# Performance work log

Hardware: AMD Instinct MI355X
Metric: run time of the kernel (lower is better)

## Reference

```python
import jax, jax.numpy as jnp
import numpy as np


def _dwconv(x, w, pad):
    # depthwise conv, NCHW, weight (C,1,kh,kw), feature_group_count=C
    return jax.lax.conv_general_dilated(
        x, w, window_strides=(1, 1), padding=pad,
        feature_group_count=x.shape[1],
        dimension_numbers=('NCHW', 'OIHW', 'NCHW'))


def _max_channel_relu(x):
    # assumed MaxChannelReLU: keep only the channel-max value at each (b,h,w)
    return x * (x == jnp.max(x, axis=1, keepdims=True))


def setup_inputs() -> dict:
    key = jax.random.key(0)
    ks = jax.random.split(key, 6)
    B, C, H, W = 16, 64, 128, 128
    x = jax.random.normal(ks[0], (B, C, H, W), dtype=jnp.float32)
    w_bbx = 0.1 * jax.random.normal(ks[1], (C, 1, 1, 1), dtype=jnp.float32)
    w_width = 0.1 * jax.random.normal(ks[2], (C, 1, 1, 11), dtype=jnp.float32)
    w_width_sh = 0.1 * jax.random.normal(ks[3], (C, 1, 1, 1), dtype=jnp.float32)
    w_height = 0.1 * jax.random.normal(ks[4], (C, 1, 11, 1), dtype=jnp.float32)
    w_height_sh = 0.1 * jax.random.normal(ks[5], (C, 1, 1, 1), dtype=jnp.float32)
    return {"x": x, "w_bbx": w_bbx, "w_width": w_width,
            "w_width_sh": w_width_sh, "w_height": w_height,
            "w_height_sh": w_height_sh}


def reference(x, w_bbx, w_width, w_width_sh, w_height, w_height_sh):
    B, C, H, W = x.shape
    # self.bbx: depthwise 1x1 conv == per-channel scale
    wh = x * w_bbx.reshape(1, C, 1, 1)
    # width branch: depthwise (1,11) conv pad 5, scaled by W, then shared 1x1
    w = _dwconv(wh, w_width, [(0, 0), (5, 5)]) * W
    w = w * w_width_sh.reshape(1, C, 1, 1)
    # height branch: depthwise (11,1) conv pad 5, scaled by H, then shared 1x1
    h = _dwconv(wh, w_height, [(5, 5), (0, 0)]) * H
    h = h * w_height_sh.reshape(1, C, 1, 1)
    sx = jax.nn.sigmoid(x)
    M = jnp.max(sx, axis=(-2, -1), keepdims=True) - 0.01
    score = x * (sx > M).astype(x.dtype)
    S = jnp.sum(score, axis=(-2, -1), keepdims=True)
    sn = score / S  # normalized weights, reused by all weighted reductions
    ws = jnp.sum(w * sn, axis=(-2, -1))
    hs = jnp.sum(h * sn, axis=(-2, -1))
    ps = jnp.max(sx, axis=(-2, -1))
    col = jnp.arange(W, dtype=x.dtype).reshape(1, 1, 1, W)
    row = jnp.arange(H, dtype=x.dtype).reshape(1, 1, H, 1)
    x1 = jnp.sum(col * sn, axis=(-2, -1)) - ws / 2
    y1 = jnp.sum(row * sn, axis=(-2, -1)) - hs / 2
    x2 = x1 + ws
    y2 = y1 + hs
    score_m = _max_channel_relu(score)
    w_m = _max_channel_relu(w)
    h_m = _max_channel_relu(h)
    i = jnp.broadcast_to(jnp.arange(B, dtype=x.dtype)[:, None], (B, C))
    bbox = jnp.stack([i, x1, y1, x2, y2, ps], axis=-1).reshape(-1, 6)
    return jnp.concatenate([score_m, w_m, h_m], axis=1), bbox
```

## Files before the change

kernel.cpp:

```cpp
#include <hip/hip_runtime.h>
#include <math.h>

#define BATCH 16
#define CH    64
#define HH    128
#define WW    128
#define PLANE (HH*WW)
#define OUT0  (BATCH*3*CH*PLANE)
#define BP    (BATCH*PLANE)

#define T_OFF   0
#define PS_OFF  1024
#define SUM_OFF 2048
#define CW_OFF  12288
#define CHS_OFF 12352
#define MAP_OFF 16384
#define FMAP_OFF 3163136

__device__ __forceinline__ float4 fmax4(float4 a, float4 b) {
    float4 r;
    r.x = fmaxf(a.x, b.x); r.y = fmaxf(a.y, b.y);
    r.z = fmaxf(a.z, b.z); r.w = fmaxf(a.w, b.w);
    return r;
}

template <int ROWS, class F>
__device__ __forceinline__ void conv_strip(const float* __restrict__ base,
                                           const float* __restrict__ wk,
                                           const float* __restrict__ hk,
                                           float cw, float chs, float T,
                                           F&& emit) {
    float4 rb[11];
#pragma unroll
    for (int r = 0; r < 11; r++)
        rb[r] = *(const float4*)(base + r * 144 + 8);
#pragma unroll
    for (int j = 0; j < ROWS; j++) {
        if (j > 0)
            rb[(j + 10) % 11] = *(const float4*)(base + (j + 10) * 144 + 8);
        float hx = 0.f, hy = 0.f, hz = 0.f, hw = 0.f;
#pragma unroll
        for (int k = 0; k < 11; k++) {
            float4 v = rb[(j + k) % 11];
            hx = fmaf(v.x, hk[k], hx);
            hy = fmaf(v.y, hk[k], hy);
            hz = fmaf(v.z, hk[k], hz);
            hw = fmaf(v.w, hk[k], hw);
        }
        float4 vx = rb[(j + 5) % 11];
        float wbuf[20];
        {
            const float* row = base + (j + 5) * 144;
            float4 a0 = *(const float4*)(row + 0);
            float4 a1 = *(const float4*)(row + 4);
            float4 a3 = *(const float4*)(row + 12);
            float4 a4 = *(const float4*)(row + 16);
            wbuf[0] = a0.x;  wbuf[1] = a0.y;  wbuf[2] = a0.z;  wbuf[3] = a0.w;
            wbuf[4] = a1.x;  wbuf[5] = a1.y;  wbuf[6] = a1.z;  wbuf[7] = a1.w;
            wbuf[8] = vx.x;  wbuf[9] = vx.y;  wbuf[10] = vx.z; wbuf[11] = vx.w;
            wbuf[12] = a3.x; wbuf[13] = a3.y; wbuf[14] = a3.z; wbuf[15] = a3.w;
            wbuf[16] = a4.x; wbuf[17] = a4.y; wbuf[18] = a4.z; wbuf[19] = a4.w;
        }
        float wo[4];
#pragma unroll
        for (int q = 0; q < 4; q++) {
            float acc = 0.f;
#pragma unroll
            for (int k = 0; k < 11; k++) acc = fmaf(wbuf[q + 3 + k], wk[k], acc);
            wo[q] = acc * cw;
        }
        float4 w4, h4, s4;
        w4.x = wo[0]; w4.y = wo[1]; w4.z = wo[2]; w4.w = wo[3];
        h4.x = hx * chs; h4.y = hy * chs; h4.z = hz * chs; h4.w = hw * chs;
        s4.x = (vx.x > T) ? vx.x : 0.f;
        s4.y = (vx.y > T) ? vx.y : 0.f;
        s4.z = (vx.z > T) ? vx.z : 0.f;
        s4.w = (vx.w > T) ? vx.w : 0.f;
        emit(j, w4, h4, s4);
    }
}

__global__ __launch_bounds__(256) void k_max(const float* __restrict__ x,
                                             const float* __restrict__ w_bbx,
                                             const float* __restrict__ w_width_sh,
                                             const float* __restrict__ w_height_sh,
                                             float* __restrict__ ws) {
    int bid = blockIdx.x;
    const float4* xp = (const float4*)(x + (size_t)bid * PLANE);
    int tid = threadIdx.x;
    float m = -INFINITY;
#pragma unroll
    for (int i = 0; i < 16; i++) {
        float4 v = xp[i * 256 + tid];
        m = fmaxf(m, fmaxf(fmaxf(v.x, v.y), fmaxf(v.z, v.w)));
    }
#pragma unroll
    for (int off = 32; off; off >>= 1) m = fmaxf(m, __shfl_xor(m, off, 64));
    __shared__ float sm[4];
    int wid = tid >> 6, lane = tid & 63;
    if (lane == 0) sm[wid] = m;
    __syncthreads();
    if (tid == 0) {
        float mm = fmaxf(fmaxf(sm[0], sm[1]), fmaxf(sm[2], sm[3]));
        float ps = 1.0f / (1.0f + expf(-mm));
        float M = ps - 0.01f;
        float T = (M > 0.0f) ? logf(M / (1.0f - M)) : -INFINITY;
        ws[T_OFF + bid] = T;
        ws[PS_OFF + bid] = ps;
    }
    if (bid < 64 && tid == 1) {
        float cb = w_bbx[bid];
        ws[CW_OFF + bid]  = 128.0f * w_width_sh[bid] * cb;
        ws[CHS_OFF + bid] = 128.0f * w_height_sh[bid] * cb;
    }
}

__global__ __launch_bounds__(256) void k_cmax(const float* __restrict__ x,
                                              const float* __restrict__ w_width,
                                              const float* __restrict__ w_height,
                                              float* __restrict__ ws) {
    __shared__ float xs[4 * 18 * 144];
    int bid = blockIdx.x;
    int band = bid & 15;
    int cg   = (bid >> 4) & 3;
    int b    = bid >> 6;
    int r0 = band * 8;
    int tid = threadIdx.x;
    int cs = tid & 31;
    int rs = (tid >> 5) & 1;
    int ig = tid >> 6;
    int slot = tid & 63;

    float4* xs4 = (float4*)xs;
    for (int i = tid; i < 4 * 18 * 36; i += 256)
        xs4[i] = make_float4(0.f, 0.f, 0.f, 0.f);

    float4 mw[4], mh[4], ms[4];
#pragma unroll
    for (int j = 0; j < 4; j++) {
        mw[j] = make_float4(-INFINITY, -INFINITY, -INFINITY, -INFINITY);
        mh[j] = mw[j];
        ms[j] = mw[j];
    }

    for (int chunk = 0; chunk < 4; chunk++) {
        int ch0 = cg * 16 + chunk * 4;
        __syncthreads();
        for (int j = tid; j < 4 * 576; j += 256) {
            int i = j / 576;
            int rem = j - i * 576;
            int lr = rem >> 5;
            int c4 = rem & 31;
            int gr = r0 - 5 + lr;
            if (gr >= 0 && gr < 128)
                *(float4*)(xs + (i * 18 + lr) * 144 + 8 + c4 * 4) =
                    *(const float4*)(x +
                        ((size_t)((b * 64 + ch0 + i) * 128 + gr)) * 128 + c4 * 4);
        }
        __syncthreads();
        int c = ch0 + ig;
        float T   = ws[T_OFF + b * 64 + c];
        float cwv = ws[CW_OFF + c];
        float chsv= ws[CHS_OFF + c];
        float wk[11], hk[11];
#pragma unroll
        for (int k = 0; k < 11; k++) {
            wk[k] = w_width[c * 11 + k];
            hk[k] = w_height[c * 11 + k];
        }
        const float* basep = xs + (ig * 18 + rs * 4) * 144 + cs * 4;
        conv_strip<4>(basep, wk, hk, cwv, chsv, T,
            [&](int j, float4 w4, float4 h4, float4 s4) {
                mw[j] = fmax4(mw[j], w4);
                mh[j] = fmax4(mh[j], h4);
                ms[j] = fmax4(ms[j], s4);
            });
    }
    __syncthreads();
    float4* cb = (float4*)xs;
    if (ig > 0) {
#pragma unroll
        for (int j = 0; j < 4; j++) {
            cb[((ig - 1) * 64 + slot) * 12 + j]     = mw[j];
            cb[((ig - 1) * 64 + slot) * 12 + 4 + j] = mh[j];
            cb[((ig - 1) * 64 + slot) * 12 + 8 + j] = ms[j];
        }
    }
    __syncthreads();
    if (ig == 0) {
#pragma unroll
        for (int g = 0; g < 3; g++) {
#pragma unroll
            for (int j = 0; j < 4; j++) {
                mw[j] = fmax4(mw[j], cb[(g * 64 + slot) * 12 + j]);
                mh[j] = fmax4(mh[j], cb[(g * 64 + slot) * 12 + 4 + j]);
                ms[j] = fmax4(ms[j], cb[(g * 64 + slot) * 12 + 8 + j]);
            }
        }
        int pbase = b * PLANE + (r0 + rs * 4) * 128 + cs * 4;
#pragma unroll
        for (int j = 0; j < 4; j++) {
            *(float4*)(ws + MAP_OFF + (size_t)(cg * 3 + 0) * BP + pbase + j * 128) = mw[j];
            *(float4*)(ws + MAP_OFF + (size_t)(cg * 3 + 1) * BP + pbase + j * 128) = mh[j];
            *(float4*)(ws + MAP_OFF + (size_t)(cg * 3 + 2) * BP + pbase + j * 128) = ms[j];
        }
    }
}

__global__ __launch_bounds__(256) void k_combine(float* __restrict__ ws) {
    int id = blockIdx.x * 256 + threadIdx.x;
    int f = id >> 16;
    int r = id & 65535;
    float4 m = *(const float4*)(ws + MAP_OFF + (size_t)f * BP + (size_t)r * 4);
#pragma unroll
    for (int g = 1; g < 4; g++) {
        float4 v = *(const float4*)(ws + MAP_OFF + (size_t)(g * 3 + f) * BP + (size_t)r * 4);
        m = fmax4(m, v);
    }
    *(float4*)(ws + FMAP_OFF + (size_t)f * BP + (size_t)r * 4) = m;
}

__global__ __launch_bounds__(256) void k_write(
    const float* __restrict__ x,
    const float* __restrict__ w_width, const float* __restrict__ w_height,
    float* __restrict__ ws, float* __restrict__ out) {
    __shared__ float xs[74 * 144];
    __shared__ float red[4 * 5];
    int bid = blockIdx.x;
    int half = bid & 1;
    int plane = bid >> 1;
    int b = plane >> 6, c = plane & 63;
    int r0 = half * 64;
    int tid = threadIdx.x;
    int cs = tid & 31;
    int rs = tid >> 5;

    float4* xs4 = (float4*)xs;
    for (int i = tid; i < 74 * 36; i += 256) xs4[i] = make_float4(0.f, 0.f, 0.f, 0.f);
    __syncthreads();
    const float* xp = x + (size_t)plane * PLANE;
    for (int j = tid; j < 74 * 32; j += 256) {
        int br = j >> 5, c4 = j & 31;
        int gr = r0 - 5 + br;
        if (gr >= 0 && gr < 128)
            *(float4*)&xs[br * 144 + 8 + c4 * 4] =
                *(const float4*)(xp + gr * 128 + c4 * 4);
    }
    float wk[11], hk[11];
#pragma unroll
    for (int k = 0; k < 11; k++) {
        wk[k] = w_width[c * 11 + k];
        hk[k] = w_height[c * 11 + k];
    }
    float T   = ws[T_OFF + plane];
    float cwv = ws[CW_OFF + c];
    float chsv= ws[CHS_OFF + c];
    __syncthreads();

    float S = 0.f, Sw = 0.f, Sh = 0.f, Scol = 0.f, Srow = 0.f;
    float* outS = out + (size_t)(b * 192 + c) * PLANE + r0 * 128;
    float* outW = out + (size_t)(b * 192 + 64 + c) * PLANE + r0 * 128;
    float* outH = out + (size_t)(b * 192 + 128 + c) * PLANE + r0 * 128;
    const float* mwp = ws + FMAP_OFF + 0 * (size_t)BP + b * PLANE + r0 * 128;
    const float* mhp = ws + FMAP_OFF + 1 * (size_t)BP + b * PLANE + r0 * 128;
    const float* msp = ws + FMAP_OFF + 2 * (size_t)BP + b * PLANE + r0 * 128;

    const float* basep = xs + (rs * 8) * 144 + cs * 4;
    conv_strip<8>(basep, wk, hk, cwv, chsv, T,
        [&](int j, float4 w4, float4 h4, float4 s4) {
            int ly = rs * 8 + j;
            int p = ly * 128 + cs * 4;
            float s4sum = s4.x + s4.y + s4.z + s4.w;
            S += s4sum;
            Srow += (float)(r0 + ly) * s4sum;
            Sw = fmaf(w4.x, s4.x, Sw); Sw = fmaf(w4.y, s4.y, Sw);
            Sw = fmaf(w4.z, s4.z, Sw); Sw = fmaf(w4.w, s4.w, Sw);
            Sh = fmaf(h4.x, s4.x, Sh); Sh = fmaf(h4.y, s4.y, Sh);
            Sh = fmaf(h4.z, s4.z, Sh); Sh = fmaf(h4.w, s4.w, Sh);
            int xc = cs * 4;
            Scol = fmaf((float)(xc + 0), s4.x, Scol);
            Scol = fmaf((float)(xc + 1), s4.y, Scol);
            Scol = fmaf((float)(xc + 2), s4.z, Scol);
            Scol = fmaf((float)(xc + 3), s4.w, Scol);

            float4 mw = *(const float4*)(mwp + p);
            float4 mh = *(const float4*)(mhp + p);
            float4 msv = *(const float4*)(msp + p);
            float4 o;
            o.x = (s4.x == msv.x) ? s4.x : 0.f;
            o.y = (s4.y == msv.y) ? s4.y : 0.f;
            o.z = (s4.z == msv.z) ? s4.z : 0.f;
            o.w = (s4.w == msv.w) ? s4.w : 0.f;
            *(float4*)(outS + p) = o;
            o.x = (w4.x == mw.x) ? w4.x : 0.f;
            o.y = (w4.y == mw.y) ? w4.y : 0.f;
            o.z = (w4.z == mw.z) ? w4.z : 0.f;
            o.w = (w4.w == mw.w) ? w4.w : 0.f;
            *(float4*)(outW + p) = o;
            o.x = (h4.x == mh.x) ? h4.x : 0.f;
            o.y = (h4.y == mh.y) ? h4.y : 0.f;
            o.z = (h4.z == mh.z) ? h4.z : 0.f;
            o.w = (h4.w == mh.w) ? h4.w : 0.f;
            *(float4*)(outH + p) = o;
        });
#pragma unroll
    for (int off = 32; off; off >>= 1) {
        S    += __shfl_xor(S, off, 64);
        Sw   += __shfl_xor(Sw, off, 64);
        Sh   += __shfl_xor(Sh, off, 64);
        Scol += __shfl_xor(Scol, off, 64);
        Srow += __shfl_xor(Srow, off, 64);
    }
    int wid = tid >> 6, lane = tid & 63;
    if (lane == 0) {
        red[wid * 5 + 0] = S;   red[wid * 5 + 1] = Sw;
        red[wid * 5 + 2] = Sh;  red[wid * 5 + 3] = Scol;
        red[wid * 5 + 4] = Srow;
    }
    __syncthreads();
    if (tid == 0) {
        float a0 = 0, a1 = 0, a2 = 0, a3 = 0, a4 = 0;
#pragma unroll
        for (int w2 = 0; w2 < 4; w2++) {
            a0 += red[w2 * 5 + 0]; a1 += red[w2 * 5 + 1];
            a2 += red[w2 * 5 + 2]; a3 += red[w2 * 5 + 3];
            a4 += red[w2 * 5 + 4];
        }
        int base = SUM_OFF + half * 5120;
        ws[base + 0 * 1024 + plane] = a0;
        ws[base + 1 * 1024 + plane] = a1;
        ws[base + 2 * 1024 + plane] = a2;
        ws[base + 3 * 1024 + plane] = a3;
        ws[base + 4 * 1024 + plane] = a4;
    }
}

__global__ __launch_bounds__(256) void k_bbox(const float* __restrict__ ws,
                                              float* __restrict__ out) {
    int idx = blockIdx.x * 256 + threadIdx.x;
    if (idx >= 1024) return;
    int b = idx >> 6;
    float S    = ws[SUM_OFF + 0 * 1024 + idx] + ws[SUM_OFF + 5120 + 0 * 1024 + idx];
    float Sw   = ws[SUM_OFF + 1 * 1024 + idx] + ws[SUM_OFF + 5120 + 1 * 1024 + idx];
    float Sh   = ws[SUM_OFF + 2 * 1024 + idx] + ws[SUM_OFF + 5120 + 2 * 1024 + idx];
    float Scol = ws[SUM_OFF + 3 * 1024 + idx] + ws[SUM_OFF + 5120 + 3 * 1024 + idx];
    float Srow = ws[SUM_OFF + 4 * 1024 + idx] + ws[SUM_OFF + 5120 + 4 * 1024 + idx];
    float ps   = ws[PS_OFF + idx];
    float inv = 1.0f / S;
    float wsv = Sw * inv, hsv = Sh * inv;
    float x1 = Scol * inv - 0.5f * wsv;
    float y1 = Srow * inv - 0.5f * hsv;
    float* o = out + OUT0 + (size_t)idx * 6;
    o[0] = (float)b;
    o[1] = x1;
    o[2] = y1;
    o[3] = x1 + wsv;
    o[4] = y1 + hsv;
    o[5] = ps;
}

extern "C" void kernel_launch(void* const* d_in, const int* in_sizes, int n_in,
                              void* d_out, int out_size, void* d_ws, size_t ws_size,
                              hipStream_t stream) {
    const float* x          = (const float*)d_in[0];
    const float* w_bbx      = (const float*)d_in[1];
    const float* w_width    = (const float*)d_in[2];
    const float* w_width_sh = (const float*)d_in[3];
    const float* w_height   = (const float*)d_in[4];
    const float* w_height_sh= (const float*)d_in[5];
    float* out = (float*)d_out;
    float* ws  = (float*)d_ws;

    k_max<<<dim3(1024), dim3(256), 0, stream>>>(x, w_bbx, w_width_sh, w_height_sh, ws);
    k_cmax<<<dim3(1024), dim3(256), 0, stream>>>(x, w_width, w_height, ws);
    k_combine<<<dim3(768), dim3(256), 0, stream>>>(ws);
    k_write<<<dim3(2048), dim3(256), 0, stream>>>(x, w_width, w_height, ws, out);
    k_bbox<<<dim3(4), dim3(256), 0, stream>>>(ws, out);
}
```

Before: 323.8 us.

## Fuse channel-max combine and bbox computation into the write kernel

Removes the separate combine kernel by having the write kernel take the max over the four partial channel-group maps directly. It also removes the bbox kernel by using an atomic block counter so the last finishing write block computes the bbox outputs. This saves two launches and the intermediate combined-map write and read. In exchange, every write block reads four times as much map data, and completion ordering now depends on threadfence plus an atomic counter.

```diff
diff --git a/kernel.cpp b/kernel.cpp
--- a/kernel.cpp
+++ b/kernel.cpp
@@ -14,8 +14,8 @@
 #define SUM_OFF 2048
 #define CW_OFF  12288
 #define CHS_OFF 12352
+#define CNT_OFF 12416
 #define MAP_OFF 16384
-#define FMAP_OFF 3163136
 
 __device__ __forceinline__ float4 fmax4(float4 a, float4 b) {
     float4 r;
@@ -113,6 +113,8 @@
         ws[CW_OFF + bid]  = 128.0f * w_width_sh[bid] * cb;
         ws[CHS_OFF + bid] = 128.0f * w_height_sh[bid] * cb;
     }
+    if (bid == 0 && tid == 2)
+        ((unsigned int*)ws)[CNT_OFF] = 0u;
 }
 
 __global__ __launch_bounds__(256) void k_cmax(const float* __restrict__ x,
@@ -207,25 +209,13 @@
     }
 }
 
-__global__ __launch_bounds__(256) void k_combine(float* __restrict__ ws) {
-    int id = blockIdx.x * 256 + threadIdx.x;
-    int f = id >> 16;
-    int r = id & 65535;
-    float4 m = *(const float4*)(ws + MAP_OFF + (size_t)f * BP + (size_t)r * 4);
-#pragma unroll
-    for (int g = 1; g < 4; g++) {
-        float4 v = *(const float4*)(ws + MAP_OFF + (size_t)(g * 3 + f) * BP + (size_t)r * 4);
-        m = fmax4(m, v);
-    }
-    *(float4*)(ws + FMAP_OFF + (size_t)f * BP + (size_t)r * 4) = m;
-}
-
 __global__ __launch_bounds__(256) void k_write(
     const float* __restrict__ x,
     const float* __restrict__ w_width, const float* __restrict__ w_height,
     float* __restrict__ ws, float* __restrict__ out) {
     __shared__ float xs[74 * 144];
     __shared__ float red[4 * 5];
+    __shared__ int lastFlag;
     int bid = blockIdx.x;
     int half = bid & 1;
     int plane = bid >> 1;
@@ -261,9 +251,7 @@
     float* outS = out + (size_t)(b * 192 + c) * PLANE + r0 * 128;
     float* outW = out + (size_t)(b * 192 + 64 + c) * PLANE + r0 * 128;
     float* outH = out + (size_t)(b * 192 + 128 + c) * PLANE + r0 * 128;
-    const float* mwp = ws + FMAP_OFF + 0 * (size_t)BP + b * PLANE + r0 * 128;
-    const float* mhp = ws + FMAP_OFF + 1 * (size_t)BP + b * PLANE + r0 * 128;
-    const float* msp = ws + FMAP_OFF + 2 * (size_t)BP + b * PLANE + r0 * 128;
+    const float* mg = ws + MAP_OFF + (size_t)b * PLANE + r0 * 128;
 
     const float* basep = xs + (rs * 8) * 144 + cs * 4;
     conv_strip<8>(basep, wk, hk, cwv, chsv, T,
@@ -283,9 +271,15 @@
             Scol = fmaf((float)(xc + 2), s4.z, Scol);
             Scol = fmaf((float)(xc + 3), s4.w, Scol);
 
-            float4 mw = *(const float4*)(mwp + p);
-            float4 mh = *(const float4*)(mhp + p);
-            float4 msv = *(const float4*)(msp + p);
+            float4 mw  = *(const float4*)(mg + (size_t)(0 * 3 + 0) * BP + p);
+            float4 mh  = *(const float4*)(mg + (size_t)(0 * 3 + 1) * BP + p);
+            float4 msv = *(const float4*)(mg + (size_t)(0 * 3 + 2) * BP + p);
+#pragma unroll
+            for (int g = 1; g < 4; g++) {
+                mw  = fmax4(mw,  *(const float4*)(mg + (size_t)(g * 3 + 0) * BP + p));
+                mh  = fmax4(mh,  *(const float4*)(mg + (size_t)(g * 3 + 1) * BP + p));
+                msv = fmax4(msv, *(const float4*)(mg + (size_t)(g * 3 + 2) * BP + p));
+            }
             float4 o;
             o.x = (s4.x == msv.x) ? s4.x : 0.f;
             o.y = (s4.y == msv.y) ? s4.y : 0.f;
@@ -332,31 +326,37 @@
         ws[base + 2 * 1024 + plane] = a2;
         ws[base + 3 * 1024 + plane] = a3;
         ws[base + 4 * 1024 + plane] = a4;
-    }
-}
-
-__global__ __launch_bounds__(256) void k_bbox(const float* __restrict__ ws,
-                                              float* __restrict__ out) {
-    int idx = blockIdx.x * 256 + threadIdx.x;
-    if (idx >= 1024) return;
-    int b = idx >> 6;
-    float S    = ws[SUM_OFF + 0 * 1024 + idx] + ws[SUM_OFF + 5120 + 0 * 1024 + idx];
-    float Sw   = ws[SUM_OFF + 1 * 1024 + idx] + ws[SUM_OFF + 5120 + 1 * 1024 + idx];
-    float Sh   = ws[SUM_OFF + 2 * 1024 + idx] + ws[SUM_OFF + 5120 + 2 * 1024 + idx];
-    float Scol = ws[SUM_OFF + 3 * 1024 + idx] + ws[SUM_OFF + 5120 + 3 * 1024 + idx];
-    float Srow = ws[SUM_OFF + 4 * 1024 + idx] + ws[SUM_OFF + 5120 + 4 * 1024 + idx];
-    float ps   = ws[PS_OFF + idx];
-    float inv = 1.0f / S;
-    float wsv = Sw * inv, hsv = Sh * inv;
-    float x1 = Scol * inv - 0.5f * wsv;
-    float y1 = Srow * inv - 0.5f * hsv;
-    float* o = out + OUT0 + (size_t)idx * 6;
-    o[0] = (float)b;
-    o[1] = x1;
-    o[2] = y1;
-    o[3] = x1 + wsv;
-    o[4] = y1 + hsv;
-    o[5] = ps;
+        __threadfence();
+        unsigned int old = atomicAdd((unsigned int*)ws + CNT_OFF, 1u);
+        lastFlag = (old == 2047u) ? 1 : 0;
+    }
+    __syncthreads();
+    if (lastFlag) {
+        __threadfence();
+        volatile const float* vws = ws;
+#pragma unroll
+        for (int k = 0; k < 4; k++) {
+            int idx = k * 256 + tid;
+            int bb = idx >> 6;
+            float Ssum = vws[SUM_OFF + 0 * 1024 + idx] + vws[SUM_OFF + 5120 + 0 * 1024 + idx];
+            float Sws  = vws[SUM_OFF + 1 * 1024 + idx] + vws[SUM_OFF + 5120 + 1 * 1024 + idx];
+            float Shs  = vws[SUM_OFF + 2 * 1024 + idx] + vws[SUM_OFF + 5120 + 2 * 1024 + idx];
+            float Scl  = vws[SUM_OFF + 3 * 1024 + idx] + vws[SUM_OFF + 5120 + 3 * 1024 + idx];
+            float Srw  = vws[SUM_OFF + 4 * 1024 + idx] + vws[SUM_OFF + 5120 + 4 * 1024 + idx];
+            float ps   = vws[PS_OFF + idx];
+            float inv = 1.0f / Ssum;
+            float wsv = Sws * inv, hsv = Shs * inv;
+            float x1 = Scl * inv - 0.5f * wsv;
+            float y1 = Srw * inv - 0.5f * hsv;
+            float* o = out + OUT0 + (size_t)idx * 6;
+            o[0] = (float)bb;
+            o[1] = x1;
+            o[2] = y1;
+            o[3] = x1 + wsv;
+            o[4] = y1 + hsv;
+            o[5] = ps;
+        }
+    }
 }
 
 extern "C" void kernel_launch(void* const* d_in, const int* in_sizes, int n_in,
@@ -373,7 +373,5 @@
 
     k_max<<<dim3(1024), dim3(256), 0, stream>>>(x, w_bbx, w_width_sh, w_height_sh, ws);
     k_cmax<<<dim3(1024), dim3(256), 0, stream>>>(x, w_width, w_height, ws);
-    k_combine<<<dim3(768), dim3(256), 0, stream>>>(ws);
     k_write<<<dim3(2048), dim3(256), 0, stream>>>(x, w_width, w_height, ws, out);
-    k_bbox<<<dim3(4), dim3(256), 0, stream>>>(ws, out);
-}
+}
```

After: 428.4 us. +32.3%, slower.
